# Kernel tuning notes

Measured on AMD Instinct MI355X. Metric: run time of the kernel, lower is better.

## Reference

```python
import jax, jax.numpy as jnp
import numpy as np

HEADS = 16
D_HEAD = 64
EPS = 1e-5


def _ln(x, g, b):
    m = jnp.mean(x, axis=-1, keepdims=True)
    v = jnp.var(x, axis=-1, keepdims=True)
    return (x - m) * jax.lax.rsqrt(v + EPS) * g + b


def _attn(xq, xc, Wq, Wk, Wv, Wo, bo):
    # Wq: [dim, inner], Wk/Wv: [ctx_dim, inner], Wo: [inner, dim]
    B, N, _ = xq.shape
    S = xc.shape[1]
    q = (xq @ Wq).reshape(B, N, HEADS, D_HEAD)
    k = (xc @ Wk).reshape(B, S, HEADS, D_HEAD)
    v = (xc @ Wv).reshape(B, S, HEADS, D_HEAD)
    scale = D_HEAD ** -0.5
    scores = jnp.einsum('bnhd,bshd->bhns', q, k) * scale
    attn = jax.nn.softmax(scores, axis=-1)
    out = jnp.einsum('bhns,bshd->bnhd', attn, v).reshape(B, N, HEADS * D_HEAD)
    return out @ Wo + bo


def _geglu_ff(x, Wp, bp, Wf, bf):
    h = x @ Wp + bp  # [B,N,2*inner]
    a, gate = jnp.split(h, 2, axis=-1)
    # torch F.gelu default is exact (erf) gelu
    return (a * jax.nn.gelu(gate, approximate=False)) @ Wf + bf


def setup_inputs() -> dict:
    key = jax.random.key(0)
    ks = jax.random.split(key, 16)
    dim, ctx, inner, ffin = 1024, 768, HEADS * D_HEAD, 4 * 1024
    def w(k, i, o):
        return jax.random.normal(k, (i, o), jnp.float32) * (i ** -0.5)
    inp = {
        'x': jax.random.normal(ks[0], (4, 2048, dim), jnp.float32),
        'context': jax.random.normal(ks[1], (4, 77, ctx), jnp.float32),
        'Wq1': w(ks[2], dim, inner), 'Wk1': w(ks[3], dim, inner), 'Wv1': w(ks[4], dim, inner),
        'Wo1': w(ks[5], inner, dim), 'bo1': jnp.zeros((dim,), jnp.float32),
        'Wq2': w(ks[6], dim, inner), 'Wk2': w(ks[7], ctx, inner), 'Wv2': w(ks[8], ctx, inner),
        'Wo2': w(ks[9], inner, dim), 'bo2': jnp.zeros((dim,), jnp.float32),
        'Wp': w(ks[10], dim, 2 * ffin), 'bp': jnp.zeros((2 * ffin,), jnp.float32),
        'Wf': w(ks[11], ffin, dim), 'bf': jnp.zeros((dim,), jnp.float32),
        'g1': jnp.ones((dim,), jnp.float32), 'b1': jnp.zeros((dim,), jnp.float32),
        'g2': jnp.ones((dim,), jnp.float32), 'b2': jnp.zeros((dim,), jnp.float32),
        'g3': jnp.ones((dim,), jnp.float32), 'b3': jnp.zeros((dim,), jnp.float32),
    }
    return inp


def reference(x, context, Wq1, Wk1, Wv1, Wo1, bo1, Wq2, Wk2, Wv2, Wo2, bo2,
              Wp, bp, Wf, bf, g1, b1, g2, b2, g3, b3):
    x = _attn(_ln(x, g1, b1), _ln(x, g1, b1), Wq1, Wk1, Wv1, Wo1, bo1) + x
    x = _attn(_ln(x, g2, b2), context, Wq2, Wk2, Wv2, Wo2, bo2) + x
    x = _geglu_ff(_ln(x, g3, b3), Wp, bp, Wf, bf) + x
    return x
```

## Files before the change

kernel.cpp:

```cpp
#include <hip/hip_runtime.h>

typedef unsigned short u16;
typedef __bf16 bf16x8 __attribute__((ext_vector_type(8)));
typedef float f32x4 __attribute__((ext_vector_type(4)));

#define HEADS 16
#define DHEAD 64
#define DIM 1024
#define NTOK 2048
#define BATCH 4
#define CTXD 768
#define SCROSS 77
#define FFIN 4096

__device__ inline float bf2f(u16 v) { return __uint_as_float(((unsigned)v) << 16); }
__device__ inline u16 f2bf(float f) {
    unsigned u = __float_as_uint(f);
    unsigned r = u + 0x7fffu + ((u >> 16) & 1u);
    return (u16)(r >> 16);
}
__device__ inline f32x4 f4zero() { f32x4 v; v[0]=0.f; v[1]=0.f; v[2]=0.f; v[3]=0.f; return v; }
__device__ inline bf16x8 as_bf16x8(uint4 u) { union { uint4 a; bf16x8 b; } c; c.a = u; return c.b; }

__device__ inline void gload_lds16(const u16* g, u16* l) {
    __builtin_amdgcn_global_load_lds((const __attribute__((address_space(1))) unsigned*)g,
                                     (__attribute__((address_space(3))) unsigned*)l, 16, 0, 0);
}

__global__ __launch_bounds__(256) void wt_k(const float* __restrict__ W, u16* __restrict__ WT,
                                            int K, int N, float scale, int remap) {
    __shared__ u16 Ts[64][72];
    int k0 = blockIdx.x * 64, n0 = blockIdx.y * 64;
    int t = threadIdx.x;
    int r = t >> 2, c4 = (t & 3) * 16;
    const float* wp = W + (size_t)(k0 + r) * N + n0 + c4;
    #pragma unroll
    for (int j = 0; j < 4; j++) {
        float4 v = *(const float4*)(wp + j * 4);
        Ts[c4 + j * 4 + 0][r] = f2bf(v.x * scale);
        Ts[c4 + j * 4 + 1][r] = f2bf(v.y * scale);
        Ts[c4 + j * 4 + 2][r] = f2bf(v.z * scale);
        Ts[c4 + j * 4 + 3][r] = f2bf(v.w * scale);
    }
    __syncthreads();
    int n = t >> 2, kc = (t & 3) * 16;
    int ng = n0 + n;
    if (remap) ng = ((ng & 4095) >> 4) * 32 + ((ng >> 12) << 4) + (ng & 15);
    u16* op = WT + (size_t)ng * K + k0 + kc;
    *(uint4*)op       = *(const uint4*)&Ts[n][kc];
    *(uint4*)(op + 8) = *(const uint4*)&Ts[n][kc + 8];
}

__global__ __launch_bounds__(256) void cvt_k(const float* __restrict__ X, u16* __restrict__ Y, int n4) {
    int i = blockIdx.x * 256 + threadIdx.x;
    if (i < n4) {
        float4 v = *(const float4*)(X + (size_t)i * 4);
        uint2 o;
        o.x = (unsigned)f2bf(v.x) | ((unsigned)f2bf(v.y) << 16);
        o.y = (unsigned)f2bf(v.z) | ((unsigned)f2bf(v.w) << 16);
        *(uint2*)(Y + (size_t)i * 4) = o;
    }
}

__global__ __launch_bounds__(256) void ln_k(const float* __restrict__ X, const float* __restrict__ G,
                                            const float* __restrict__ Bt, u16* __restrict__ Y) {
    int row = blockIdx.x;
    int t = threadIdx.x;
    int w = t >> 6, lane = t & 63;
    float4 xv = *(const float4*)(X + (size_t)row * DIM + t * 4);
    float s = xv.x + xv.y + xv.z + xv.w;
    float s2 = xv.x*xv.x + xv.y*xv.y + xv.z*xv.z + xv.w*xv.w;
    for (int off = 1; off < 64; off <<= 1) {
        s  += __shfl_xor(s,  off, 64);
        s2 += __shfl_xor(s2, off, 64);
    }
    __shared__ float rs[4], rs2[4];
    if (lane == 0) { rs[w] = s; rs2[w] = s2; }
    __syncthreads();
    float S_ = rs[0] + rs[1] + rs[2] + rs[3];
    float S2_ = rs2[0] + rs2[1] + rs2[2] + rs2[3];
    float mean = S_ * (1.0f / DIM);
    float var = fmaxf(S2_ * (1.0f / DIM) - mean * mean, 0.f);
    float rstd = rsqrtf(var + 1e-5f);
    int col = t * 4;
    float4 g = *(const float4*)(G + col);
    float4 b = *(const float4*)(Bt + col);
    float y0 = (xv.x - mean) * rstd * g.x + b.x;
    float y1 = (xv.y - mean) * rstd * g.y + b.y;
    float y2 = (xv.z - mean) * rstd * g.z + b.z;
    float y3 = (xv.w - mean) * rstd * g.w + b.w;
    uint2 o;
    o.x = (unsigned)f2bf(y0) | ((unsigned)f2bf(y1) << 16);
    o.y = (unsigned)f2bf(y2) | ((unsigned)f2bf(y3) << 16);
    *(uint2*)(Y + (size_t)row * DIM + col) = o;
}

template<typename TC, bool RESID>
__global__ __launch_bounds__(256) void gemm128(const u16* __restrict__ A, int lda,
                                               const u16* __restrict__ BT,
                                               const float* __restrict__ bias, const float* resid,
                                               TC* C, int ldc, int M, int N, int K) {
    __shared__ __align__(16) u16 As[128 * 32];
    __shared__ __align__(16) u16 Bs[128 * 32];
    int m0 = blockIdx.x * 128, n0 = blockIdx.y * 128;
    int t = threadIdx.x;
    int w = t >> 6, lane = t & 63;
    int quad = lane >> 4, l16 = lane & 15;
    int mh = (w & 1) * 64, nh = (w >> 1) * 64;
    f32x4 acc[4][4];
    #pragma unroll
    for (int i = 0; i < 4; i++)
        #pragma unroll
        for (int j = 0; j < 4; j++) acc[i][j] = f4zero();
    int sr = t >> 2;
    int sc8 = (((t & 3) ^ ((sr >> 1) & 3)) * 8);
    int ra0 = min(m0 + sr, M - 1);
    int ra1 = min(m0 + sr + 64, M - 1);
    const u16* ga0 = A + (size_t)ra0 * lda + sc8;
    const u16* ga1 = A + (size_t)ra1 * lda + sc8;
    const u16* gb0 = BT + (size_t)(n0 + sr) * K + sc8;
    const u16* gb1 = BT + (size_t)(n0 + sr + 64) * K + sc8;
    u16* lA0 = &As[w * 512];
    u16* lA1 = &As[2048 + w * 512];
    u16* lB0 = &Bs[w * 512];
    u16* lB1 = &Bs[2048 + w * 512];
    int rq = ((quad ^ ((l16 >> 1) & 3)) * 8);
    for (int k0 = 0; k0 < K; k0 += 32) {
        __syncthreads();
        gload_lds16(ga0 + k0, lA0);
        gload_lds16(ga1 + k0, lA1);
        gload_lds16(gb0 + k0, lB0);
        gload_lds16(gb1 + k0, lB1);
        __syncthreads();
        bf16x8 af[4], bfv[4];
        #pragma unroll
        for (int i = 0; i < 4; i++) {
            af[i]  = as_bf16x8(*(const uint4*)&As[(mh + i * 16 + l16) * 32 + rq]);
            bfv[i] = as_bf16x8(*(const uint4*)&Bs[(nh + i * 16 + l16) * 32 + rq]);
        }
        #pragma unroll
        for (int i = 0; i < 4; i++)
            #pragma unroll
            for (int j = 0; j < 4; j++)
                acc[i][j] = __builtin_amdgcn_mfma_f32_16x16x32_bf16(af[i], bfv[j], acc[i][j], 0, 0, 0);
    }
    #pragma unroll
    for (int j = 0; j < 4; j++) {
        int gn = n0 + nh + j * 16 + l16;
        float bv = bias ? bias[gn] : 0.f;
        #pragma unroll
        for (int i = 0; i < 4; i++) {
            #pragma unroll
            for (int r = 0; r < 4; r++) {
                int gm = m0 + mh + i * 16 + quad * 4 + r;
                if (gm < M) {
                    float v = acc[i][j][r] + bv;
                    if constexpr (RESID) v += resid[(size_t)gm * N + gn];
                    if constexpr (__is_same(TC, u16)) C[(size_t)gm * ldc + gn] = f2bf(v);
                    else                              C[(size_t)gm * ldc + gn] = v;
                }
            }
        }
    }
}


#define BAR() __builtin_amdgcn_s_barrier()
#define SB0() __builtin_amdgcn_sched_barrier(0)
#define PRIO1() __builtin_amdgcn_s_setprio(1)
#define PRIO0() __builtin_amdgcn_s_setprio(0)
#define WAIT_VM6() asm volatile("s_waitcnt vmcnt(6)" ::: "memory")
#define WAIT_VM4() asm volatile("s_waitcnt vmcnt(4)" ::: "memory")
#define WAIT_VM0() asm volatile("s_waitcnt vmcnt(0)" ::: "memory")
#define WAIT_LGKM0() asm volatile("s_waitcnt lgkmcnt(0)" ::: "memory")
#define WAIT_LGKM8() asm volatile("s_waitcnt lgkmcnt(8)" ::: "memory")

#define STAGE_A_R(P, h, q, TAU) gload_lds16(gA + (size_t)((h) * 128 + (q) * 64) * 1024 + (TAU) * 64, \
                                            lA + (P) * 16384 + (h) * 8192 + (q) * 4096)
#define STAGE_B_R(P, h, q, TAU) gload_lds16(gB + (size_t)((h) * 128 + (q) * 64) * 1024 + (TAU) * 64, \
                                            lB + (P) * 16384 + (h) * 8192 + (q) * 4096)
#define RD_A(P, fi, ks) as_bf16x8(*(const uint4*)(rdA + (P) * 32768 + (fi) * 2048 + ((ks) ? o1 : o0)))
#define RD_B(P, fj, ks) as_bf16x8(*(const uint4*)(rdB + (P) * 32768 + (fj) * 2048 + ((ks) ? o1 : o0)))
#define MM(ai, aj, av, bv) acc[ai][aj] = __builtin_amdgcn_mfma_f32_16x16x32_bf16(av, bv, acc[ai][aj], 0, 0, 0)

#define Q00() do { \
    MM(0,0,A0r[0][0],B0r[0][0]); MM(1,0,A0r[1][0],B0r[0][0]); MM(2,0,A0r[2][0],B0r[0][0]); MM(3,0,A0r[3][0],B0r[0][0]); \
    MM(0,1,A0r[0][0],B0r[1][0]); MM(1,1,A0r[1][0],B0r[1][0]); MM(2,1,A0r[2][0],B0r[1][0]); MM(3,1,A0r[3][0],B0r[1][0]); \
    MM(0,0,A0r[0][1],B0r[0][1]); MM(1,0,A0r[1][1],B0r[0][1]); MM(2,0,A0r[2][1],B0r[0][1]); MM(3,0,A0r[3][1],B0r[0][1]); \
    MM(0,1,A0r[0][1],B0r[1][1]); MM(1,1,A0r[1][1],B0r[1][1]); MM(2,1,A0r[2][1],B0r[1][1]); MM(3,1,A0r[3][1],B0r[1][1]); \
} while (0)
#define Q01() do { \
    MM(0,2,A0r[0][0],B1r[0][0]); MM(1,2,A0r[1][0],B1r[0][0]); MM(2,2,A0r[2][0],B1r[0][0]); MM(3,2,A0r[3][0],B1r[0][0]); \
    MM(0,3,A0r[0][0],B1r[1][0]); MM(1,3,A0r[1][0],B1r[1][0]); MM(2,3,A0r[2][0],B1r[1][0]); MM(3,3,A0r[3][0],B1r[1][0]); \
    MM(0,2,A0r[0][1],B1r[0][1]); MM(1,2,A0r[1][1],B1r[0][1]); MM(2,2,A0r[2][1],B1r[0][1]); MM(3,2,A0r[3][1],B1r[0][1]); \
    MM(0,3,A0r[0][1],B1r[1][1]); MM(1,3,A0r[1][1],B1r[1][1]); MM(2,3,A0r[2][1],B1r[1][1]); MM(3,3,A0r[3][1],B1r[1][1]); \
} while (0)
#define Q10() do { \
    MM(4,0,A1r[0][0],B0r[0][0]); MM(5,0,A1r[1][0],B0r[0][0]); MM(6,0,A1r[2][0],B0r[0][0]); MM(7,0,A1r[3][0],B0r[0][0]); \
    MM(4,1,A1r[0][0],B0r[1][0]); MM(5,1,A1r[1][0],B0r[1][0]); MM(6,1,A1r[2][0],B0r[1][0]); MM(7,1,A1r[3][0],B0r[1][0]); \
    MM(4,0,A1r[0][1],B0r[0][1]); MM(5,0,A1r[1][1],B0r[0][1]); MM(6,0,A1r[2][1],B0r[0][1]); MM(7,0,A1r[3][1],B0r[0][1]); \
    MM(4,1,A1r[0][1],B0r[1][1]); MM(5,1,A1r[1][1],B0r[1][1]); MM(6,1,A1r[2][1],B0r[1][1]); MM(7,1,A1r[3][1],B0r[1][1]); \
} while (0)
#define Q11() do { \
    MM(4,2,A1r[0][0],B1r[0][0]); MM(5,2,A1r[1][0],B1r[0][0]); MM(6,2,A1r[2][0],B1r[0][0]); MM(7,2,A1r[3][0],B1r[0][0]); \
    MM(4,3,A1r[0][0],B1r[1][0]); MM(5,3,A1r[1][0],B1r[1][0]); MM(6,3,A1r[2][0],B1r[1][0]); MM(7,3,A1r[3][0],B1r[1][0]); \
    MM(4,2,A1r[0][1],B1r[0][1]); MM(5,2,A1r[1][1],B1r[0][1]); MM(6,2,A1r[2][1],B1r[0][1]); MM(7,2,A1r[3][1],B1r[0][1]); \
    MM(4,3,A1r[0][1],B1r[1][1]); MM(5,3,A1r[1][1],B1r[1][1]); MM(6,3,A1r[2][1],B1r[1][1]); MM(7,3,A1r[3][1],B1r[1][1]); \
} while (0)

#define TILEX(P, S0, S1, T, MIDW, ENDW, LAST) do {                                    \
       \
    B1r[0][0] = RD_B(P, 2, 0); B1r[0][1] = RD_B(P, 2, 1);                             \
    B1r[1][0] = RD_B(P, 3, 0); B1r[1][1] = RD_B(P, 3, 1);                             \
    if (S0) { STAGE_B_R((P) ^ 1, 1, 0, (T) + 1); STAGE_B_R((P) ^ 1, 1, 1, (T) + 1); } \
    SB0(); PRIO1(); Q00(); PRIO0(); SB0();                                            \
                 \
    A1r[0][0] = RD_A(P, 4, 0); A1r[0][1] = RD_A(P, 4, 1);                             \
    A1r[1][0] = RD_A(P, 5, 0); A1r[1][1] = RD_A(P, 5, 1);                             \
    A1r[2][0] = RD_A(P, 6, 0); A1r[2][1] = RD_A(P, 6, 1);                             \
    A1r[3][0] = RD_A(P, 7, 0); A1r[3][1] = RD_A(P, 7, 1);                             \
    if (S1) { STAGE_A_R(P, 0, 0, (T) + 2); STAGE_A_R(P, 1, 0, (T) + 2); }             \
    WAIT_LGKM8(); SB0(); PRIO1(); Q01(); PRIO0(); SB0();                              \
        \
    WAIT_LGKM0();                                                                     \
    if (!(LAST)) { MIDW; BAR(); }                                                     \
    SB0();                                                                            \
                \
    if (!(LAST)) {                                                                    \
        A0r[0][0] = RD_A((P) ^ 1, 0, 0); A0r[0][1] = RD_A((P) ^ 1, 0, 1);             \
        A0r[1][0] = RD_A((P) ^ 1, 1, 0); A0r[1][1] = RD_A((P) ^ 1, 1, 1);             \
        A0r[2][0] = RD_A((P) ^ 1, 2, 0); A0r[2][1] = RD_A((P) ^ 1, 2, 1);             \
        A0r[3][0] = RD_A((P) ^ 1, 3, 0); A0r[3][1] = RD_A((P) ^ 1, 3, 1);             \
    }                                                                                 \
    if (S1) { STAGE_B_R(P, 0, 0, (T) + 2); STAGE_B_R(P, 0, 1, (T) + 2); }             \
    SB0(); PRIO1(); Q10(); PRIO0(); SB0();                                            \
                                \
    if (!(LAST)) {                                                                    \
        B0r[0][0] = RD_B((P) ^ 1, 0, 0); B0r[0][1] = RD_B((P) ^ 1, 0, 1);             \
        B0r[1][0] = RD_B((P) ^ 1, 1, 0); B0r[1][1] = RD_B((P) ^ 1, 1, 1);             \
    }                                                                                 \
       \
    if (S1) { STAGE_A_R(P, 0, 1, (T) + 2); STAGE_A_R(P, 1, 1, (T) + 2); }             \
    SB0(); PRIO1(); Q11(); PRIO0(); SB0();                                            \
    if (!(LAST)) { WAIT_LGKM0(); ENDW; BAR(); }                                       \
    SB0();                                                                            \
} while (0)

template<int NBY, int LDC, int EPI>
__global__ __launch_bounds__(512, 2) void gemm256(const u16* __restrict__ A,
                                                  const u16* __restrict__ BT,
                                                  const float* __restrict__ bias,
                                                  u16* __restrict__ C) {
    __shared__ __align__(16) u16 As[2][16384];
    __shared__ __align__(16) u16 Bs[2][16384];
    int t = threadIdx.x;
    int w = t >> 6, lane = t & 63;
    int quad = lane >> 4, l16 = lane & 15;
    int wm = w >> 2, wn = w & 3;
    int bid = blockIdx.x;
    int cpx = (int)gridDim.x >> 3;
    int swz = (bid & 7) * cpx + (bid >> 3);
    int bx = swz / NBY, by = swz % NBY;
    int m0 = bx << 8, n0 = by << 8;

    int ar = t >> 3;
    int ac = (((t & 7) ^ (ar & 7)) << 3);
    const u16* gA = A + (size_t)(m0 + ar) * 1024 + ac;
    const u16* gB = BT + (size_t)(n0 + ar) * 1024 + ac;
    u16* lA = &As[0][0] + (w << 9);
    u16* lB = &Bs[0][0] + (w << 9);
    const char* rdA = (const char*)&As[0][0] + (((wm << 7) + l16) << 7);
    const char* rdB = (const char*)&Bs[0][0] + (((wn << 6) + l16) << 7);
    int o0 = (quad << 4) ^ ((l16 & 7) << 4);
    int o1 = o0 ^ 64;

    f32x4 acc[8][4];
    #pragma unroll
    for (int i = 0; i < 8; i++)
        #pragma unroll
        for (int j = 0; j < 4; j++) acc[i][j] = f4zero();

    STAGE_A_R(0, 0, 0, 0); STAGE_A_R(0, 1, 0, 0);
    STAGE_B_R(0, 0, 0, 0); STAGE_B_R(0, 0, 1, 0);
    STAGE_A_R(0, 0, 1, 0); STAGE_A_R(0, 1, 1, 0);
    STAGE_B_R(0, 1, 0, 0); STAGE_B_R(0, 1, 1, 0);
    STAGE_A_R(1, 0, 0, 1); STAGE_A_R(1, 1, 0, 1);
    STAGE_B_R(1, 0, 0, 1); STAGE_B_R(1, 0, 1, 1);
    STAGE_A_R(1, 0, 1, 1); STAGE_A_R(1, 1, 1, 1);
    WAIT_VM6();
    BAR();
    bf16x8 A0r[4][2], A1r[4][2], B0r[2][2], B1r[2][2];
    A0r[0][0] = RD_A(0, 0, 0); A0r[0][1] = RD_A(0, 0, 1);
    A0r[1][0] = RD_A(0, 1, 0); A0r[1][1] = RD_A(0, 1, 1);
    A0r[2][0] = RD_A(0, 2, 0); A0r[2][1] = RD_A(0, 2, 1);
    A0r[3][0] = RD_A(0, 3, 0); A0r[3][1] = RD_A(0, 3, 1);
    B0r[0][0] = RD_B(0, 0, 0); B0r[0][1] = RD_B(0, 0, 1);
    B0r[1][0] = RD_B(0, 1, 0); B0r[1][1] = RD_B(0, 1, 1);
    WAIT_LGKM0();
    BAR();

    #pragma unroll 1
    for (int tt = 0; tt < 14; tt += 2) {
        TILEX(0, 1, 1, tt,     WAIT_VM6(), WAIT_VM6(), 0);
        TILEX(1, 1, 1, tt + 1, WAIT_VM6(), WAIT_VM6(), 0);
    }
    TILEX(0, 1, 0, 14, WAIT_VM4(), WAIT_VM0(), 0);
    TILEX(1, 0, 0, 15, (void)0, (void)0, 1);

    if constexpr (EPI == 0) {
        int gm0 = m0 + wm * 128 + quad * 4;
        int gn0 = n0 + wn * 64 + l16;
        #pragma unroll
        for (int fi = 0; fi < 8; fi++)
            #pragma unroll
            for (int fj = 0; fj < 4; fj++)
                #pragma unroll
                for (int r = 0; r < 4; r++)
                    C[(size_t)(gm0 + fi * 16 + r) * LDC + gn0 + fj * 16] = f2bf(acc[fi][fj][r]);
    } else {
        int gm0 = m0 + wm * 128 + quad * 4;
        int oc0 = (n0 >> 1) + wn * 32 + l16;
        #pragma unroll
        for (int jp = 0; jp < 2; jp++) {
            int oc = oc0 + jp * 16;
            float ba = bias[oc];
            float bg = bias[FFIN + oc];
            #pragma unroll
            for (int fi = 0; fi < 8; fi++)
                #pragma unroll
                for (int r = 0; r < 4; r++) {
                    float a = acc[fi][2 * jp][r] + ba;
                    float g = acc[fi][2 * jp + 1][r] + bg;
                    float v = a * (0.5f * g * (1.f + erff(g * 0.70710678118654752f)));
                    C[(size_t)(gm0 + fi * 16 + r) * LDC + oc] = f2bf(v);
                }
        }
    }
}

__global__ __launch_bounds__(256) void attn_k(const u16* Q, int ldq, const u16* __restrict__ K,
                                              const u16* __restrict__ V, int ldkv,
                                              u16* O, int S) {
    __shared__ __align__(16) u16 Ksh[128 * 64];
    __shared__ __align__(16) u16 Vt[64 * 128];
    __shared__ __align__(16) u16 Pb[4][16 * 128];
    int bh = blockIdx.x;
    int b = bh >> 4, h = bh & 15;
    int q0 = blockIdx.y * 64;
    int t = threadIdx.x;
    int w = t >> 6, lane = t & 63;
    int quad = lane >> 4, l16 = lane & 15;
    int sw = (l16 & 7) << 3;
    const u16* Qp = Q + ((size_t)b * NTOK + q0) * ldq + h * DHEAD;
    const u16* Kp = K + (size_t)b * S * ldkv + h * DHEAD;
    const u16* Vp = V + (size_t)b * S * ldkv + h * DHEAD;
    bf16x8 qf[2];
    #pragma unroll
    for (int ds = 0; ds < 2; ds++)
        qf[ds] = as_bf16x8(*(const uint4*)(Qp + (size_t)(w * 16 + l16) * ldq + ds * 32 + quad * 8));
    float l_l = 0.f;
    f32x4 o_acc[4];
    #pragma unroll
    for (int dt = 0; dt < 4; dt++) o_acc[dt] = f4zero();
    int kr8 = lane >> 3;
    int ksl = ((lane & 7) ^ kr8) * 8;
    int vd = (t >> 5) * 8;
    int vk = (t & 31) * 4;
    int nkt = (S + 127) / 128;
    for (int kt = 0; kt < nkt; kt++) {
        int kbase = kt * 128;
        bool full = (kbase + 128) <= S;
        __syncthreads();
        #pragma unroll
        for (int i = 0; i < 4; i++) {
            int r = min(kbase + (i * 4 + w) * 8 + kr8, S - 1);
            gload_lds16(Kp + (size_t)r * ldkv + ksl, &Ksh[(i * 4 + w) * 512]);
        }
        {
            union { uint4 u; u16 e[8]; } vr[4];
            #pragma unroll
            for (int j = 0; j < 4; j++) {
                int key = min(kbase + vk + j, S - 1);
                vr[j].u = *(const uint4*)(Vp + (size_t)key * ldkv + vd);
            }
            #pragma unroll
            for (int d = 0; d < 8; d++) {
                int row = vd + d;
                uint2 p;
                p.x = (unsigned)vr[0].e[d] | ((unsigned)vr[1].e[d] << 16);
                p.y = (unsigned)vr[2].e[d] | ((unsigned)vr[3].e[d] << 16);
                *(uint2*)&Vt[row * 128 + (vk ^ ((row & 7) << 3))] = p;
            }
        }
        __syncthreads();
        f32x4 sc[8];
        PRIO1();
        #pragma unroll
        for (int sub = 0; sub < 8; sub++) {
            const u16* kr = &Ksh[(sub * 16 + l16) * 64];
            bf16x8 kf0 = as_bf16x8(*(const uint4*)(kr + ((quad * 8) ^ sw)));
            bf16x8 kf1 = as_bf16x8(*(const uint4*)(kr + ((32 + quad * 8) ^ sw)));
            f32x4 s = __builtin_amdgcn_mfma_f32_16x16x32_bf16(kf0, qf[0], f4zero(), 0, 0, 0);
            sc[sub] = __builtin_amdgcn_mfma_f32_16x16x32_bf16(kf1, qf[1], s, 0, 0, 0);
        }
        PRIO0();
        if (!full) {
            #pragma unroll
            for (int sub = 0; sub < 8; sub++)
                #pragma unroll
                for (int r = 0; r < 4; r++)
                    if (kbase + sub * 16 + quad * 4 + r >= S) sc[sub][r] = -1e30f;
        }
        float psum = 0.f;
        #pragma unroll
        for (int sub = 0; sub < 8; sub++) {
            float p0 = __builtin_amdgcn_exp2f(sc[sub][0]);
            float p1 = __builtin_amdgcn_exp2f(sc[sub][1]);
            float p2 = __builtin_amdgcn_exp2f(sc[sub][2]);
            float p3 = __builtin_amdgcn_exp2f(sc[sub][3]);
            psum += (p0 + p1) + (p2 + p3);
            uint2 pk;
            pk.x = __builtin_amdgcn_perm(__float_as_uint(p1), __float_as_uint(p0), 0x07060302);
            pk.y = __builtin_amdgcn_perm(__float_as_uint(p3), __float_as_uint(p2), 0x07060302);
            *(uint2*)&Pb[w][l16 * 128 + ((sub * 16 + quad * 4) ^ sw)] = pk;
        }
        l_l += psum;
        PRIO1();
        #pragma unroll
        for (int kk = 0; kk < 4; kk++) {
            bf16x8 pf = as_bf16x8(*(const uint4*)&Pb[w][l16 * 128 + ((kk * 32 + quad * 8) ^ sw)]);
            #pragma unroll
            for (int dt = 0; dt < 4; dt++) {
                bf16x8 vf = as_bf16x8(*(const uint4*)&Vt[(dt * 16 + l16) * 128 + ((kk * 32 + quad * 8) ^ sw)]);
                o_acc[dt] = __builtin_amdgcn_mfma_f32_16x16x32_bf16(pf, vf, o_acc[dt], 0, 0, 0);
            }
        }
        PRIO0();
    }
    float l_tot = l_l;
    l_tot += __shfl_xor(l_tot, 16, 64);
    l_tot += __shfl_xor(l_tot, 32, 64);
    #pragma unroll
    for (int r = 0; r < 4; r++) {
        float lr = __shfl(l_tot, quad * 4 + r, 64);
        float invl = (lr > 0.f) ? (1.f / lr) : 0.f;
        int gq = q0 + w * 16 + quad * 4 + r;
        #pragma unroll
        for (int dt = 0; dt < 4; dt++) {
            O[((size_t)b * NTOK + gq) * ldq + h * DHEAD + dt * 16 + l16] = f2bf(o_acc[dt][r] * invl);
        }
    }
}

extern "C" void kernel_launch(void* const* d_in, const int* in_sizes, int n_in,
                              void* d_out, int out_size, void* d_ws, size_t ws_size,
                              hipStream_t stream) {
    const float* x   = (const float*)d_in[0];
    const float* ctx = (const float*)d_in[1];
    const float* Wq1 = (const float*)d_in[2];
    const float* Wk1 = (const float*)d_in[3];
    const float* Wv1 = (const float*)d_in[4];
    const float* Wo1 = (const float*)d_in[5];
    const float* bo1 = (const float*)d_in[6];
    const float* Wq2 = (const float*)d_in[7];
    const float* Wk2 = (const float*)d_in[8];
    const float* Wv2 = (const float*)d_in[9];
    const float* Wo2 = (const float*)d_in[10];
    const float* bo2 = (const float*)d_in[11];
    const float* Wp  = (const float*)d_in[12];
    const float* bp  = (const float*)d_in[13];
    const float* Wf  = (const float*)d_in[14];
    const float* bfb = (const float*)d_in[15];
    const float* g1  = (const float*)d_in[16];
    const float* b1  = (const float*)d_in[17];
    const float* g2  = (const float*)d_in[18];
    const float* b2  = (const float*)d_in[19];
    const float* g3  = (const float*)d_in[20];
    const float* b3  = (const float*)d_in[21];
    float* out = (float*)d_out;

    const int M = BATCH * NTOK;
    const int Mc = BATCH * SCROSS;
    u16* ws = (u16*)d_ws;
    size_t o = 0;
    u16* WqT1 = ws + o; o += (size_t)DIM * DIM;
    u16* WkT1 = ws + o; o += (size_t)DIM * DIM;
    u16* WvT1 = ws + o; o += (size_t)DIM * DIM;
    u16* WoT1 = ws + o; o += (size_t)DIM * DIM;
    u16* WqT2 = ws + o; o += (size_t)DIM * DIM;
    u16* WoT2 = ws + o; o += (size_t)DIM * DIM;
    u16* WkT2 = ws + o; o += (size_t)DIM * CTXD;
    u16* WvT2 = ws + o; o += (size_t)DIM * CTXD;
    u16* WpT  = ws + o; o += (size_t)(2 * FFIN) * DIM;
    u16* WfT  = ws + o; o += (size_t)DIM * FFIN;
    u16* ctxb = ws + o; o += (size_t)Mc * CTXD;
    u16* KVc  = ws + o; o += (size_t)Mc * 2048;
    u16* P    = ws + o; o += (size_t)M * DIM;
    u16* QKV  = ws + o; o += (size_t)M * 3072;
    u16* reg2 = ws + o; o += (size_t)M * DIM * 2;
    float* X1 = (float*)reg2;
    u16* gb = QKV;

    dim3 blk(256);
    const float qscale = 0.125f * 1.4426950408889634f;

    wt_k<<<dim3(16, 16), blk, 0, stream>>>(Wq1, WqT1, DIM, DIM, qscale, 0);
    wt_k<<<dim3(16, 16), blk, 0, stream>>>(Wk1, WkT1, DIM, DIM, 1.f, 0);
    wt_k<<<dim3(16, 16), blk, 0, stream>>>(Wv1, WvT1, DIM, DIM, 1.f, 0);
    wt_k<<<dim3(16, 16), blk, 0, stream>>>(Wo1, WoT1, DIM, DIM, 1.f, 0);
    wt_k<<<dim3(16, 16), blk, 0, stream>>>(Wq2, WqT2, DIM, DIM, qscale, 0);
    wt_k<<<dim3(16, 16), blk, 0, stream>>>(Wo2, WoT2, DIM, DIM, 1.f, 0);
    wt_k<<<dim3(12, 16), blk, 0, stream>>>(Wk2, WkT2, CTXD, DIM, 1.f, 0);
    wt_k<<<dim3(12, 16), blk, 0, stream>>>(Wv2, WvT2, CTXD, DIM, 1.f, 0);
    wt_k<<<dim3(16, 128), blk, 0, stream>>>(Wp, WpT, DIM, 2 * FFIN, 1.f, 1);
    wt_k<<<dim3(64, 16), blk, 0, stream>>>(Wf, WfT, FFIN, DIM, 1.f, 0);
    cvt_k<<<dim3((Mc * CTXD / 4 + 255) / 256), blk, 0, stream>>>(ctx, ctxb, Mc * CTXD / 4);

    ln_k<<<dim3(M), blk, 0, stream>>>(x, g1, b1, P);
    gemm256<12, 3072, 0><<<dim3(32 * 12), dim3(512), 0, stream>>>(P, WqT1, nullptr, QKV);
    attn_k<<<dim3(BATCH * HEADS, NTOK / 64), blk, 0, stream>>>(
        QKV, 3072, QKV + 1024, QKV + 2048, 3072, QKV, NTOK);
    gemm128<float, true><<<dim3(M / 128, DIM / 128), blk, 0, stream>>>(
        QKV, 3072, WoT1, bo1, x, X1, DIM, M, DIM, DIM);

    ln_k<<<dim3(M), blk, 0, stream>>>(X1, g2, b2, P);
    gemm128<u16, false><<<dim3(M / 128, DIM / 128), blk, 0, stream>>>(
        P, DIM, WqT2, nullptr, nullptr, QKV, 3072, M, DIM, DIM);
    gemm128<u16, false><<<dim3((Mc + 127) / 128, 2048 / 128), blk, 0, stream>>>(
        ctxb, CTXD, WkT2, nullptr, nullptr, KVc, 2048, Mc, 2048, CTXD);
    attn_k<<<dim3(BATCH * HEADS, NTOK / 64), blk, 0, stream>>>(
        QKV, 3072, KVc, KVc + 1024, 2048, QKV, SCROSS);
    gemm128<float, true><<<dim3(M / 128, DIM / 128), blk, 0, stream>>>(
        QKV, 3072, WoT2, bo2, X1, out, DIM, M, DIM, DIM);

    ln_k<<<dim3(M), blk, 0, stream>>>(out, g3, b3, P);
    gemm256<32, 4096, 1><<<dim3(32 * 32), dim3(512), 0, stream>>>(P, WpT, bp, gb);
    gemm128<float, true><<<dim3(M / 128, DIM / 128), blk, 0, stream>>>(
        gb, FFIN, WfT, bfb, out, out, DIM, M, DIM, FFIN);
}
```

Baseline: 873.9 us.

## Restructure GEMM main loop into barrier-separated four-phase schedule per tile

Replaces the software-pipelined tile macro, which prefetched the next tile's A0/B0 fragments across iterations, with a schedule where each tile loads its own fragments and every MFMA quadrant is bracketed by workgroup barriers. This aims to keep waves in lockstep so LDS reads and global-to-LDS staging interleave predictably with the matrix cores. It adds eight barriers per tile and drops the cross-tile register prefetch, so LDS latency may be exposed more often. The vmcnt waits are also adjusted for the final tiles.

```diff
diff --git a/kernel.cpp b/kernel.cpp
--- a/kernel.cpp
+++ b/kernel.cpp
@@ -170,7 +170,6 @@
 #define PRIO1() __builtin_amdgcn_s_setprio(1)
 #define PRIO0() __builtin_amdgcn_s_setprio(0)
 #define WAIT_VM6() asm volatile("s_waitcnt vmcnt(6)" ::: "memory")
-#define WAIT_VM4() asm volatile("s_waitcnt vmcnt(4)" ::: "memory")
 #define WAIT_VM0() asm volatile("s_waitcnt vmcnt(0)" ::: "memory")
 #define WAIT_LGKM0() asm volatile("s_waitcnt lgkmcnt(0)" ::: "memory")
 #define WAIT_LGKM8() asm volatile("s_waitcnt lgkmcnt(8)" ::: "memory")
@@ -208,42 +207,37 @@
     MM(4,3,A1r[0][1],B1r[1][1]); MM(5,3,A1r[1][1],B1r[1][1]); MM(6,3,A1r[2][1],B1r[1][1]); MM(7,3,A1r[3][1],B1r[1][1]); \
 } while (0)
 
-#define TILEX(P, S0, S1, T, MIDW, ENDW, LAST) do {                                    \
-       \
+#define TILEM(P, S0, S1, T, PH3W, HASW) do {                                          \
+                                     \
+    A0r[0][0] = RD_A(P, 0, 0); A0r[0][1] = RD_A(P, 0, 1);                             \
+    A0r[1][0] = RD_A(P, 1, 0); A0r[1][1] = RD_A(P, 1, 1);                             \
+    A0r[2][0] = RD_A(P, 2, 0); A0r[2][1] = RD_A(P, 2, 1);                             \
+    A0r[3][0] = RD_A(P, 3, 0); A0r[3][1] = RD_A(P, 3, 1);                             \
+    B0r[0][0] = RD_B(P, 0, 0); B0r[0][1] = RD_B(P, 0, 1);                             \
+    B0r[1][0] = RD_B(P, 1, 0); B0r[1][1] = RD_B(P, 1, 1);                             \
+    if (S0) { STAGE_B_R((P) ^ 1, 1, 0, (T) + 1); STAGE_B_R((P) ^ 1, 1, 1, (T) + 1); } \
+    WAIT_LGKM8();                                                                     \
+    BAR(); WAIT_LGKM0(); SB0();                                                       \
+    PRIO1(); Q00(); PRIO0(); SB0(); BAR();                                            \
+                                             \
     B1r[0][0] = RD_B(P, 2, 0); B1r[0][1] = RD_B(P, 2, 1);                             \
     B1r[1][0] = RD_B(P, 3, 0); B1r[1][1] = RD_B(P, 3, 1);                             \
-    if (S0) { STAGE_B_R((P) ^ 1, 1, 0, (T) + 1); STAGE_B_R((P) ^ 1, 1, 1, (T) + 1); } \
-    SB0(); PRIO1(); Q00(); PRIO0(); SB0();                                            \
-                 \
+    if (S1) { STAGE_A_R(P, 0, 0, (T) + 2); STAGE_A_R(P, 1, 0, (T) + 2); }             \
+    BAR(); WAIT_LGKM0(); SB0();                                                       \
+    PRIO1(); Q01(); PRIO0(); SB0(); BAR();                                            \
+                                             \
     A1r[0][0] = RD_A(P, 4, 0); A1r[0][1] = RD_A(P, 4, 1);                             \
     A1r[1][0] = RD_A(P, 5, 0); A1r[1][1] = RD_A(P, 5, 1);                             \
     A1r[2][0] = RD_A(P, 6, 0); A1r[2][1] = RD_A(P, 6, 1);                             \
     A1r[3][0] = RD_A(P, 7, 0); A1r[3][1] = RD_A(P, 7, 1);                             \
-    if (S1) { STAGE_A_R(P, 0, 0, (T) + 2); STAGE_A_R(P, 1, 0, (T) + 2); }             \
-    WAIT_LGKM8(); SB0(); PRIO1(); Q01(); PRIO0(); SB0();                              \
-        \
-    WAIT_LGKM0();                                                                     \
-    if (!(LAST)) { MIDW; BAR(); }                                                     \
-    SB0();                                                                            \
-                \
-    if (!(LAST)) {                                                                    \
-        A0r[0][0] = RD_A((P) ^ 1, 0, 0); A0r[0][1] = RD_A((P) ^ 1, 0, 1);             \
-        A0r[1][0] = RD_A((P) ^ 1, 1, 0); A0r[1][1] = RD_A((P) ^ 1, 1, 1);             \
-        A0r[2][0] = RD_A((P) ^ 1, 2, 0); A0r[2][1] = RD_A((P) ^ 1, 2, 1);             \
-        A0r[3][0] = RD_A((P) ^ 1, 3, 0); A0r[3][1] = RD_A((P) ^ 1, 3, 1);             \
-    }                                                                                 \
     if (S1) { STAGE_B_R(P, 0, 0, (T) + 2); STAGE_B_R(P, 0, 1, (T) + 2); }             \
-    SB0(); PRIO1(); Q10(); PRIO0(); SB0();                                            \
-                                \
-    if (!(LAST)) {                                                                    \
-        B0r[0][0] = RD_B((P) ^ 1, 0, 0); B0r[0][1] = RD_B((P) ^ 1, 0, 1);             \
-        B0r[1][0] = RD_B((P) ^ 1, 1, 0); B0r[1][1] = RD_B((P) ^ 1, 1, 1);             \
-    }                                                                                 \
-       \
+    BAR(); WAIT_LGKM0(); SB0();                                                       \
+    PRIO1(); Q10(); PRIO0(); SB0(); BAR();                                            \
+                     \
     if (S1) { STAGE_A_R(P, 0, 1, (T) + 2); STAGE_A_R(P, 1, 1, (T) + 2); }             \
-    SB0(); PRIO1(); Q11(); PRIO0(); SB0();                                            \
-    if (!(LAST)) { WAIT_LGKM0(); ENDW; BAR(); }                                       \
-    SB0();                                                                            \
+    if (HASW) { PH3W; }                                                               \
+    BAR(); SB0();                                                                     \
+    PRIO1(); Q11(); PRIO0(); SB0(); BAR();                                            \
 } while (0)
 
 template<int NBY, int LDC, int EPI>
@@ -289,23 +283,15 @@
     STAGE_A_R(1, 0, 1, 1); STAGE_A_R(1, 1, 1, 1);
     WAIT_VM6();
     BAR();
+
     bf16x8 A0r[4][2], A1r[4][2], B0r[2][2], B1r[2][2];
-    A0r[0][0] = RD_A(0, 0, 0); A0r[0][1] = RD_A(0, 0, 1);
-    A0r[1][0] = RD_A(0, 1, 0); A0r[1][1] = RD_A(0, 1, 1);
-    A0r[2][0] = RD_A(0, 2, 0); A0r[2][1] = RD_A(0, 2, 1);
-    A0r[3][0] = RD_A(0, 3, 0); A0r[3][1] = RD_A(0, 3, 1);
-    B0r[0][0] = RD_B(0, 0, 0); B0r[0][1] = RD_B(0, 0, 1);
-    B0r[1][0] = RD_B(0, 1, 0); B0r[1][1] = RD_B(0, 1, 1);
-    WAIT_LGKM0();
-    BAR();
-
     #pragma unroll 1
     for (int tt = 0; tt < 14; tt += 2) {
-        TILEX(0, 1, 1, tt,     WAIT_VM6(), WAIT_VM6(), 0);
-        TILEX(1, 1, 1, tt + 1, WAIT_VM6(), WAIT_VM6(), 0);
-    }
-    TILEX(0, 1, 0, 14, WAIT_VM4(), WAIT_VM0(), 0);
-    TILEX(1, 0, 0, 15, (void)0, (void)0, 1);
+        TILEM(0, 1, 1, tt,     WAIT_VM6(), 1);
+        TILEM(1, 1, 1, tt + 1, WAIT_VM6(), 1);
+    }
+    TILEM(0, 1, 0, 14, WAIT_VM0(), 1);
+    TILEM(1, 0, 0, 15, (void)0, 0);
 
     if constexpr (EPI == 0) {
         int gm0 = m0 + wm * 128 + quad * 4;
```

After: 918.4 us. +5.1%, slower.
